# Kernel tuning notes

Measured on AMD Instinct MI355X. Metric: run time of the kernel, lower is better.

Reference implementation:

```python
import jax, jax.numpy as jnp
import numpy as np

N_NODES = 100000
N_EDGES = 1600000
N_GRAPHS = 1024
D = 128
L = 3
BN_EPS = 1e-5


def setup_inputs() -> dict:
    key = jax.random.key(0)
    ks = jax.random.split(key, 16)
    x = jax.random.normal(ks[0], (N_NODES, D), dtype=jnp.float32)
    edge_index = jax.random.randint(ks[1], (2, N_EDGES), 0, N_NODES, dtype=jnp.int64)
    batch = jnp.sort(jax.random.randint(ks[2], (N_NODES,), 0, N_GRAPHS, dtype=jnp.int64))
    w = lambda k, shape: jax.random.normal(k, shape, dtype=jnp.float32) * 0.05
    return {
        "x": x,
        "edge_index": edge_index,
        "batch": batch,
        "conv_W1": w(ks[3], (L, D, D)),
        "conv_b1": w(ks[4], (L, D)),
        "bn_gamma": jax.random.uniform(ks[5], (L, D), dtype=jnp.float32) + 0.5,
        "bn_beta": w(ks[6], (L, D)),
        "bn_mean": w(ks[7], (L, D)),
        "bn_var": jax.random.uniform(ks[8], (L, D), dtype=jnp.float32) + 0.5,
        "conv_W2": w(ks[9], (L, D, D)),
        "conv_b2": w(ks[10], (L, D)),
        "head_W1": w(ks[11], (D, D)),
        "head_b1": w(ks[12], (D,)),
        "head_W2": w(ks[13], (D, D)),
        "head_b2": w(ks[14], (D,)),
    }


def reference(x, edge_index, batch, conv_W1, conv_b1, bn_gamma, bn_beta,
              bn_mean, bn_var, conv_W2, conv_b2, head_W1, head_b1,
              head_W2, head_b2):
    n = x.shape[0]
    src, dst = edge_index[0], edge_index[1]
    for l in range(L):
        # GINConv, eps=0: nn(x + sum_{j->i} x_j)
        agg = jax.ops.segment_sum(x[src], dst, num_segments=n)  # [N, D]
        h = x + agg
        # MLP([in, h, h]): Linear -> BatchNorm(eval) -> ReLU -> Linear
        h = h @ conv_W1[l] + conv_b1[l]
        h = (h - bn_mean[l]) * jax.lax.rsqrt(bn_var[l] + BN_EPS) * bn_gamma[l] + bn_beta[l]
        h = jax.nn.relu(h)
        h = h @ conv_W2[l] + conv_b2[l]
        x = jax.nn.relu(h)  # .relu() in the outer forward
    # global_add_pool over graph ids
    g = jax.ops.segment_sum(x, batch, num_segments=N_GRAPHS)  # [B, D]
    # head MLP (norm=None, dropout inactive at eval): Linear -> ReLU -> Linear
    g = jax.nn.relu(g @ head_W1 + head_b1)
    return g @ head_W2 + head_b2
```

## Files before the change

kernel.cpp:

```cpp
#include <hip/hip_runtime.h>

#define N_NODES  100000
#define N_EDGES  1600000
#define N_GRAPHS 1024
#define D        128
#define BN_EPS   1e-5f

#define FNSLICE      98
#define FSLICE_NODES 1024
#define FSLICE_CAP   20480
#define QCAP         96
#define CCHUNK       4000
#define CGRID        400

#define CVT_BLOCKS   6250
#define PW_BLOCKS    384
#define FOLD_BLOCKS  3
#define GST_BLOCKS   5
#define MISC_BASE    (CVT_BLOCKS + PW_BLOCKS + FOLD_BLOCKS + GST_BLOCKS)
#define COMPACT_BASE (MISC_BASE + 1)
#define SETUP_GRID   (COMPACT_BASE + CGRID)

#define GATHER_GRID  12500

typedef short bf16x8 __attribute__((ext_vector_type(8)));
typedef float f32x4  __attribute__((ext_vector_type(4)));

__device__ __forceinline__ ushort f2bf(float f) {
    unsigned int b = __float_as_uint(f);
    return (ushort)((b + 0x7fffu + ((b >> 16) & 1u)) >> 16);
}
__device__ __forceinline__ float bflo(unsigned int u) { return __uint_as_float(u << 16); }
__device__ __forceinline__ float bfhi(unsigned int u) { return __uint_as_float(u & 0xffff0000u); }
__device__ __forceinline__ unsigned int packbf(float x, float y) {
    return (unsigned int)f2bf(x) | ((unsigned int)f2bf(y) << 16);
}

__global__ __launch_bounds__(256) void setup_kernel(
        const float* __restrict__ x, ushort* __restrict__ xb,
        const float* __restrict__ W1, const float* __restrict__ W2,
        ushort* __restrict__ Wt,
        const float* __restrict__ b1, const float* __restrict__ gamma,
        const float* __restrict__ beta, const float* __restrict__ mean,
        const float* __restrict__ var, const float* __restrict__ b2,
        float* __restrict__ folds,
        const int* __restrict__ batch, int* __restrict__ gstart,
        int* __restrict__ slice_tail, int* __restrict__ offsets,
        const int* __restrict__ src, const int* __restrict__ dst,
        unsigned int* __restrict__ squeue) {
    __shared__ unsigned int qbuf[FNSLICE * QCAP];
    __shared__ int qcnt[FNSLICE];
    __shared__ int qbase[FNSLICE];
    int b = blockIdx.x, t = threadIdx.x;
    if (b < CVT_BLOCKS) {
        size_t i = ((size_t)b * 256 + t) * 8;
        float4 v0 = *(const float4*)(x + i);
        float4 v1 = *(const float4*)(x + i + 4);
        uint4 o;
        o.x = packbf(v0.x, v0.y); o.y = packbf(v0.z, v0.w);
        o.z = packbf(v1.x, v1.y); o.w = packbf(v1.z, v1.w);
        *(uint4*)(xb + i) = o;
    } else if (b < CVT_BLOCKS + PW_BLOCKS) {
        int idx = (b - CVT_BLOCKS) * 256 + t;
        int i = idx >> 14, r = idx & 16383;
        int n = r >> 7, k = r & 127, l = i >> 1;
        const float* W = (i & 1) ? (W2 + (size_t)l * D * D) : (W1 + (size_t)l * D * D);
        Wt[idx] = f2bf(W[k * D + n]);
    } else if (b < CVT_BLOCKS + PW_BLOCKS + FOLD_BLOCKS) {
        int idx = (b - CVT_BLOCKS - PW_BLOCKS) * 256 + t;
        if (idx < 6 * D) {
            int i = idx >> 7, j = idx & 127, l = i >> 1;
            float s, o;
            if ((i & 1) == 0) {
                float sv = gamma[l * D + j] * rsqrtf(var[l * D + j] + BN_EPS);
                s = sv;
                o = (b1[l * D + j] - mean[l * D + j]) * sv + beta[l * D + j];
            } else {
                s = 1.0f;
                o = b2[l * D + j];
            }
            folds[(size_t)i * 2 * D + j]     = s;
            folds[(size_t)i * 2 * D + D + j] = o;
        }
    } else if (b < MISC_BASE) {
        int g = (b - CVT_BLOCKS - PW_BLOCKS - FOLD_BLOCKS) * 256 + t;
        if (g <= N_GRAPHS) {
            int lo = 0, hi = N_NODES;
            while (lo < hi) {
                int mid = (lo + hi) >> 1;
                if (batch[mid] < g) lo = mid + 1; else hi = mid;
            }
            gstart[g] = lo;
        }
    } else if (b == MISC_BASE) {
        if (t == 255) offsets[N_NODES] = N_EDGES;
    } else {
        for (int i = t; i < FNSLICE; i += 256) qcnt[i] = 0;
        __syncthreads();
        int e0 = (b - COMPACT_BASE) * CCHUNK;
        int eend = e0 + CCHUNK; if (eend > N_EDGES) eend = N_EDGES;
        for (int e = e0 + t; e < eend; e += 256) {
            int d = dst[e], s = src[e];
            int sl = d >> 10;
            unsigned int pk = ((unsigned int)(d & 1023) << 17) | (unsigned int)s;
            int pos = atomicAdd(&qcnt[sl], 1);
            if (pos < QCAP) qbuf[sl * QCAP + pos] = pk;
            else {
                int gp = atomicAdd(&slice_tail[sl], 1);
                squeue[(size_t)sl * FSLICE_CAP + gp] = pk;
            }
        }
        __syncthreads();
        for (int i = t; i < FNSLICE; i += 256) {
            int n = qcnt[i]; if (n > QCAP) n = QCAP;
            qbase[i] = atomicAdd(&slice_tail[i], n);
        }
        __syncthreads();
        int wv = t >> 6, ln = t & 63;
        for (int sl = wv; sl < FNSLICE; sl += 4) {
            int n = qcnt[sl]; if (n > QCAP) n = QCAP;
            int gb = qbase[sl];
            for (int i = ln; i < n; i += 64)
                squeue[(size_t)sl * FSLICE_CAP + gb + i] = qbuf[sl * QCAP + i];
        }
    }
}

__global__ __launch_bounds__(1024) void fill_local(const unsigned int* __restrict__ squeue,
                                                   const int* __restrict__ slice_tail,
                                                   int* __restrict__ offsets,
                                                   int* __restrict__ csr_src) {
    __shared__ int hist[FSLICE_NODES];
    __shared__ int cur[FSLICE_NODES];
    __shared__ int sbase[128];
    __shared__ int wsum[16];
    int sl = blockIdx.x, t = threadIdx.x;
    int n = slice_tail[sl];
    if (t < 128) sbase[t] = (t < FNSLICE) ? slice_tail[t] : 0;
    hist[t] = 0;
    __syncthreads();
    for (int off = 1; off < 128; off <<= 1) {
        int u = (t < 128 && t >= off) ? sbase[t - off] : 0;
        __syncthreads();
        if (t < 128) sbase[t] += u;
        __syncthreads();
    }
    int gbase = (sl == 0) ? 0 : sbase[sl - 1];
    size_t qb = (size_t)sl * FSLICE_CAP;
    for (int i = t; i < n; i += 1024)
        atomicAdd(&hist[squeue[qb + i] >> 17], 1);
    __syncthreads();
    int c = hist[t];
    int lane = t & 63, w = t >> 6;
    int sc = c;
#pragma unroll
    for (int off = 1; off < 64; off <<= 1) {
        int u = __shfl_up(sc, off, 64);
        if (lane >= off) sc += u;
    }
    if (lane == 63) wsum[w] = sc;
    __syncthreads();
    if (t < 16) {
        int ws = wsum[t];
        int s2 = ws;
#pragma unroll
        for (int off = 1; off < 16; off <<= 1) {
            int u = __shfl_up(s2, off, 16);
            if (t >= off) s2 += u;
        }
        wsum[t] = s2 - ws;
    }
    __syncthreads();
    int gslot = gbase + sc + wsum[w] - c;
    cur[t] = gslot;
    int node = sl * FSLICE_NODES + t;
    if (node < N_NODES) offsets[node] = gslot;
    __syncthreads();
    for (int i = t; i < n; i += 1024) {
        unsigned int p = squeue[qb + i];
        int slot = atomicAdd(&cur[p >> 17], 1);
        csr_src[slot] = (int)(p & 0x1FFFFu);
    }
}

__device__ __forceinline__ void drain_stream(const unsigned int* __restrict__ base,
                                             const int* __restrict__ csr,
                                             int i, int e, int lane,
                                             float& ax, float& ay) {
    for (; i + 15 < e; i += 16) {
        int s0 = csr[i],      s1 = csr[i + 1],  s2 = csr[i + 2],  s3 = csr[i + 3];
        int s4 = csr[i + 4],  s5 = csr[i + 5],  s6 = csr[i + 6],  s7 = csr[i + 7];
        int s8 = csr[i + 8],  s9 = csr[i + 9],  sa = csr[i + 10], sb = csr[i + 11];
        int sc = csr[i + 12], sd = csr[i + 13], se = csr[i + 14], sf = csr[i + 15];
        unsigned int v0 = base[(size_t)s0 * 64 + lane];
        unsigned int v1 = base[(size_t)s1 * 64 + lane];
        unsigned int v2 = base[(size_t)s2 * 64 + lane];
        unsigned int v3 = base[(size_t)s3 * 64 + lane];
        unsigned int v4 = base[(size_t)s4 * 64 + lane];
        unsigned int v5 = base[(size_t)s5 * 64 + lane];
        unsigned int v6 = base[(size_t)s6 * 64 + lane];
        unsigned int v7 = base[(size_t)s7 * 64 + lane];
        unsigned int v8 = base[(size_t)s8 * 64 + lane];
        unsigned int v9 = base[(size_t)s9 * 64 + lane];
        unsigned int va = base[(size_t)sa * 64 + lane];
        unsigned int vb = base[(size_t)sb * 64 + lane];
        unsigned int vc = base[(size_t)sc * 64 + lane];
        unsigned int vd = base[(size_t)sd * 64 + lane];
        unsigned int ve = base[(size_t)se * 64 + lane];
        unsigned int vf = base[(size_t)sf * 64 + lane];
        ax += bflo(v0) + bflo(v1) + bflo(v2) + bflo(v3)
            + bflo(v4) + bflo(v5) + bflo(v6) + bflo(v7)
            + bflo(v8) + bflo(v9) + bflo(va) + bflo(vb)
            + bflo(vc) + bflo(vd) + bflo(ve) + bflo(vf);
        ay += bfhi(v0) + bfhi(v1) + bfhi(v2) + bfhi(v3)
            + bfhi(v4) + bfhi(v5) + bfhi(v6) + bfhi(v7)
            + bfhi(v8) + bfhi(v9) + bfhi(va) + bfhi(vb)
            + bfhi(vc) + bfhi(vd) + bfhi(ve) + bfhi(vf);
    }
    for (; i + 3 < e; i += 4) {
        int s0 = csr[i], s1 = csr[i + 1], s2 = csr[i + 2], s3 = csr[i + 3];
        unsigned int v0 = base[(size_t)s0 * 64 + lane];
        unsigned int v1 = base[(size_t)s1 * 64 + lane];
        unsigned int v2 = base[(size_t)s2 * 64 + lane];
        unsigned int v3 = base[(size_t)s3 * 64 + lane];
        ax += bflo(v0) + bflo(v1) + bflo(v2) + bflo(v3);
        ay += bfhi(v0) + bfhi(v1) + bfhi(v2) + bfhi(v3);
    }
    for (; i < e; ++i) {
        unsigned int v = base[(size_t)csr[i] * 64 + lane];
        ax += bflo(v); ay += bfhi(v);
    }
}

__global__ __launch_bounds__(256) void gather_bf16(const ushort* __restrict__ xb,
                                                   const int* __restrict__ offsets,
                                                   const int* __restrict__ csr_src,
                                                   ushort* __restrict__ hb) {
    int wv = threadIdx.x >> 6, lane = threadIdx.x & 63;
    int n0 = (blockIdx.x * 4 + wv) * 2;
    const unsigned int* base = (const unsigned int*)xb;
    unsigned int u0 = base[(size_t)n0 * 64 + lane];
    unsigned int u1 = base[(size_t)(n0 + 1) * 64 + lane];
    float ax0 = bflo(u0), ay0 = bfhi(u0);
    float ax1 = bflo(u1), ay1 = bfhi(u1);
    int i0 = offsets[n0];
    int e0 = offsets[n0 + 1];
    int i1 = e0;
    int e1 = offsets[n0 + 2];
    while (i0 + 7 < e0 && i1 + 7 < e1) {
        int s0 = csr_src[i0],     s1 = csr_src[i0 + 1],
            s2 = csr_src[i0 + 2], s3 = csr_src[i0 + 3];
        int s4 = csr_src[i0 + 4], s5 = csr_src[i0 + 5],
            s6 = csr_src[i0 + 6], s7 = csr_src[i0 + 7];
        int r0 = csr_src[i1],     r1 = csr_src[i1 + 1],
            r2 = csr_src[i1 + 2], r3 = csr_src[i1 + 3];
        int r4 = csr_src[i1 + 4], r5 = csr_src[i1 + 5],
            r6 = csr_src[i1 + 6], r7 = csr_src[i1 + 7];
        unsigned int v0 = base[(size_t)s0 * 64 + lane];
        unsigned int v1 = base[(size_t)s1 * 64 + lane];
        unsigned int v2 = base[(size_t)s2 * 64 + lane];
        unsigned int v3 = base[(size_t)s3 * 64 + lane];
        unsigned int v4 = base[(size_t)s4 * 64 + lane];
        unsigned int v5 = base[(size_t)s5 * 64 + lane];
        unsigned int v6 = base[(size_t)s6 * 64 + lane];
        unsigned int v7 = base[(size_t)s7 * 64 + lane];
        unsigned int w0 = base[(size_t)r0 * 64 + lane];
        unsigned int w1 = base[(size_t)r1 * 64 + lane];
        unsigned int w2 = base[(size_t)r2 * 64 + lane];
        unsigned int w3 = base[(size_t)r3 * 64 + lane];
        unsigned int w4 = base[(size_t)r4 * 64 + lane];
        unsigned int w5 = base[(size_t)r5 * 64 + lane];
        unsigned int w6 = base[(size_t)r6 * 64 + lane];
        unsigned int w7 = base[(size_t)r7 * 64 + lane];
        ax0 += bflo(v0) + bflo(v1) + bflo(v2) + bflo(v3)
             + bflo(v4) + bflo(v5) + bflo(v6) + bflo(v7);
        ay0 += bfhi(v0) + bfhi(v1) + bfhi(v2) + bfhi(v3)
             + bfhi(v4) + bfhi(v5) + bfhi(v6) + bfhi(v7);
        ax1 += bflo(w0) + bflo(w1) + bflo(w2) + bflo(w3)
             + bflo(w4) + bflo(w5) + bflo(w6) + bflo(w7);
        ay1 += bfhi(w0) + bfhi(w1) + bfhi(w2) + bfhi(w3)
             + bfhi(w4) + bfhi(w5) + bfhi(w6) + bfhi(w7);
        i0 += 8; i1 += 8;
    }
    drain_stream(base, csr_src, i0, e0, lane, ax0, ay0);
    drain_stream(base, csr_src, i1, e1, lane, ax1, ay1);
    ((unsigned int*)hb)[(size_t)n0 * 64 + lane]       = packbf(ax0, ay0);
    ((unsigned int*)hb)[(size_t)(n0 + 1) * 64 + lane] = packbf(ax1, ay1);
}

__global__ __launch_bounds__(512, 4) void fused_gemm(const ushort* __restrict__ in,
                                                     ushort* __restrict__ out,
                                                     const ushort* __restrict__ Wt1,
                                                     const ushort* __restrict__ Wt2,
                                                     const float* __restrict__ fold1,
                                                     const float* __restrict__ fold2) {
    __shared__ ushort As[128 * 136];
    __shared__ ushort Bs[128 * 136];
    int t = threadIdx.x;
    int row0 = blockIdx.x * 128;

#pragma unroll
    for (int i = 0; i < 4; ++i) {
        int f = t + 512 * i; int m = f >> 4, g = f & 15;
        *(float4*)(As + m * 136 + g * 8) = *(const float4*)(in + (size_t)(row0 + m) * D + g * 8);
        *(float4*)(Bs + m * 136 + g * 8) = *(const float4*)(Wt1 + (size_t)m * D + g * 8);
    }
    const uint4* w2v = (const uint4*)Wt2;
    uint4 p0 = w2v[t];
    uint4 p1 = w2v[t + 512];
    uint4 p2 = w2v[t + 1024];
    uint4 p3 = w2v[t + 1536];
    __syncthreads();

    int lane = t & 63, wv = t >> 6;
    int quad = lane >> 4, mr = lane & 15;
    int mbase = wv * 16;
    const ushort* ap = As + (mbase + mr) * 136 + quad * 8;
    bf16x8 a0 = *(const bf16x8*)(ap);
    bf16x8 a1 = *(const bf16x8*)(ap + 32);
    bf16x8 a2 = *(const bf16x8*)(ap + 64);
    bf16x8 a3 = *(const bf16x8*)(ap + 96);

#pragma unroll
    for (int nt = 0; nt < 8; ++nt) {
        const ushort* bq = Bs + (nt * 16 + mr) * 136 + quad * 8;
        bf16x8 b0 = *(const bf16x8*)(bq);
        bf16x8 b1 = *(const bf16x8*)(bq + 32);
        bf16x8 b2 = *(const bf16x8*)(bq + 64);
        bf16x8 b3 = *(const bf16x8*)(bq + 96);
        f32x4 acc = {0.f, 0.f, 0.f, 0.f};
        acc = __builtin_amdgcn_mfma_f32_16x16x32_bf16(a0, b0, acc, 0, 0, 0);
        acc = __builtin_amdgcn_mfma_f32_16x16x32_bf16(a1, b1, acc, 0, 0, 0);
        acc = __builtin_amdgcn_mfma_f32_16x16x32_bf16(a2, b2, acc, 0, 0, 0);
        acc = __builtin_amdgcn_mfma_f32_16x16x32_bf16(a3, b3, acc, 0, 0, 0);
        int j = nt * 16 + mr;
        float s = fold1[j], o = fold1[D + j];
#pragma unroll
        for (int r = 0; r < 4; ++r) {
            float z = fmaxf(fmaf(acc[r], s, o), 0.0f);
            As[(mbase + quad * 4 + r) * 136 + j] = f2bf(z);
        }
    }
    __syncthreads();

    {
        int f0 = t;          *(uint4*)(Bs + (f0 >> 4) * 136 + (f0 & 15) * 8) = p0;
        int f1 = t + 512;    *(uint4*)(Bs + (f1 >> 4) * 136 + (f1 & 15) * 8) = p1;
        int f2 = t + 1024;   *(uint4*)(Bs + (f2 >> 4) * 136 + (f2 & 15) * 8) = p2;
        int f3 = t + 1536;   *(uint4*)(Bs + (f3 >> 4) * 136 + (f3 & 15) * 8) = p3;
    }
    const ushort* hp = As + (mbase + mr) * 136 + quad * 8;
    bf16x8 h0 = *(const bf16x8*)(hp);
    bf16x8 h1 = *(const bf16x8*)(hp + 32);
    bf16x8 h2 = *(const bf16x8*)(hp + 64);
    bf16x8 h3 = *(const bf16x8*)(hp + 96);
    __syncthreads();

#pragma unroll
    for (int nt = 0; nt < 8; ++nt) {
        const ushort* bq = Bs + (nt * 16 + mr) * 136 + quad * 8;
        bf16x8 b0 = *(const bf16x8*)(bq);
        bf16x8 b1 = *(const bf16x8*)(bq + 32);
        bf16x8 b2 = *(const bf16x8*)(bq + 64);
        bf16x8 b3 = *(const bf16x8*)(bq + 96);
        f32x4 acc = {0.f, 0.f, 0.f, 0.f};
        acc = __builtin_amdgcn_mfma_f32_16x16x32_bf16(h0, b0, acc, 0, 0, 0);
        acc = __builtin_amdgcn_mfma_f32_16x16x32_bf16(h1, b1, acc, 0, 0, 0);
        acc = __builtin_amdgcn_mfma_f32_16x16x32_bf16(h2, b2, acc, 0, 0, 0);
        acc = __builtin_amdgcn_mfma_f32_16x16x32_bf16(h3, b3, acc, 0, 0, 0);
        int j = nt * 16 + mr;
        float o = fold2[D + j];
#pragma unroll
        for (int r = 0; r < 4; ++r) {
            float z = fmaxf(acc[r] + o, 0.0f);
            As[(mbase + quad * 4 + r) * 136 + j] = f2bf(z);
        }
    }
    __syncthreads();

#pragma unroll
    for (int i = 0; i < 8; ++i) {
        int f = t + 512 * i; int lr = f >> 5, g = f & 31;
        if (row0 + lr < N_NODES)
            *(float2*)(out + (size_t)(row0 + lr) * D + g * 4) =
                *(const float2*)(As + lr * 136 + g * 4);
    }
}

__global__ __launch_bounds__(128) void poolhead_kernel(const ushort* __restrict__ xb,
                                                       const int* __restrict__ gstart,
                                                       const float* __restrict__ W1,
                                                       const float* __restrict__ b1,
                                                       const float* __restrict__ W2,
                                                       const float* __restrict__ b2,
                                                       float* __restrict__ out) {
    __shared__ float row[128];
    __shared__ float t1[128];
    int r = blockIdx.x, j = threadIdx.x;
    float acc = 0.0f;
    int b = gstart[r], e = gstart[r + 1];
    for (int i = b; i < e; ++i)
        acc += __uint_as_float(((unsigned int)xb[(size_t)i * D + j]) << 16);
    row[j] = acc;
    __syncthreads();
    float a1 = b1[j];
    for (int k = 0; k < D; ++k) a1 = fmaf(row[k], W1[k * D + j], a1);
    t1[j] = fmaxf(a1, 0.0f);
    __syncthreads();
    float a2 = b2[j];
    for (int k = 0; k < D; ++k) a2 = fmaf(t1[k], W2[k * D + j], a2);
    out[r * D + j] = a2;
}

extern "C" void kernel_launch(void* const* d_in, const int* in_sizes, int n_in,
                              void* d_out, int out_size, void* d_ws, size_t ws_size,
                              hipStream_t stream) {
    const float* x        = (const float*)d_in[0];
    const int*   ei       = (const int*)d_in[1];
    const int*   src      = ei;
    const int*   dst      = ei + N_EDGES;
    const int*   batch    = (const int*)d_in[2];
    const float* conv_W1  = (const float*)d_in[3];
    const float* conv_b1  = (const float*)d_in[4];
    const float* bn_gamma = (const float*)d_in[5];
    const float* bn_beta  = (const float*)d_in[6];
    const float* bn_mean  = (const float*)d_in[7];
    const float* bn_var   = (const float*)d_in[8];
    const float* conv_W2  = (const float*)d_in[9];
    const float* conv_b2  = (const float*)d_in[10];
    const float* head_W1  = (const float*)d_in[11];
    const float* head_b1  = (const float*)d_in[12];
    const float* head_W2  = (const float*)d_in[13];
    const float* head_b2  = (const float*)d_in[14];
    float* out = (float*)d_out;

    char* ws = (char*)d_ws;
    size_t off = 0;
    auto alloc = [&](size_t bytes) -> void* {
        void* p = ws + off;
        off = (off + bytes + 255) & ~(size_t)255;
        return p;
    };
    const size_t NODE_BUF = (size_t)(N_NODES + 128) * D * sizeof(ushort);
    ushort* buf0    = (ushort*)alloc(NODE_BUF);
    ushort* buf1    = (ushort*)alloc(NODE_BUF);
    ushort* Wt      = (ushort*)alloc((size_t)6 * D * D * sizeof(ushort));
    float*  folds   = (float*)alloc((size_t)6 * 2 * D * sizeof(float));
    unsigned int* squeue = (unsigned int*)alloc((size_t)FNSLICE * FSLICE_CAP * sizeof(unsigned int));
    int*   csr_src  = (int*)alloc((size_t)(N_EDGES + 64) * sizeof(int));
    int*   offsets  = (int*)alloc((size_t)(N_NODES + 1) * sizeof(int));
    int*   slice_tail = (int*)alloc((size_t)FNSLICE * sizeof(int));
    int*   gstart   = (int*)alloc((size_t)(N_GRAPHS + 1) * sizeof(int));

    hipMemsetAsync(slice_tail, 0, FNSLICE * sizeof(int), stream);
    setup_kernel<<<SETUP_GRID, 256, 0, stream>>>(
        x, buf0, conv_W1, conv_W2, Wt,
        conv_b1, bn_gamma, bn_beta, bn_mean, bn_var, conv_b2, folds,
        batch, gstart, slice_tail, offsets, src, dst, squeue);
    fill_local<<<FNSLICE, 1024, 0, stream>>>(squeue, slice_tail, offsets, csr_src);

    const int FUSED_GRID = (N_NODES + 127) / 128;
    for (int l = 0; l < 3; ++l) {
        gather_bf16<<<GATHER_GRID, 256, 0, stream>>>(buf0, offsets, csr_src, buf1);
        fused_gemm<<<FUSED_GRID, 512, 0, stream>>>(buf1, buf0,
            Wt + (size_t)(2 * l) * D * D, Wt + (size_t)(2 * l + 1) * D * D,
            folds + (size_t)(2 * l) * 2 * D, folds + (size_t)(2 * l + 1) * 2 * D);
    }

    poolhead_kernel<<<N_GRAPHS, 128, 0, stream>>>(buf0, gstart, head_W1, head_b1,
                                                  head_W2, head_b2, out);
}
```

Baseline: 439.6 us.

## Fuse global add pooling into last layer GEMM epilogue via atomics

The last GIN layer's GEMM now accumulates its output rows directly into a per-graph pool buffer with run-length segmented sums and float atomics, instead of writing node features and reading them back in the pool/head kernel. The setup kernel zeroes the pool buffer instead of binary-searching graph start offsets, and the head kernel just reads pooled rows. This removes the final node-feature write and reread and the serial per-graph reduction loop. In exchange it adds atomic contention and makes the float summation order nondeterministic.

```diff
diff --git a/kernel.cpp b/kernel.cpp
--- a/kernel.cpp
+++ b/kernel.cpp
@@ -16,8 +16,9 @@
 #define CVT_BLOCKS   6250
 #define PW_BLOCKS    384
 #define FOLD_BLOCKS  3
-#define GST_BLOCKS   5
-#define MISC_BASE    (CVT_BLOCKS + PW_BLOCKS + FOLD_BLOCKS + GST_BLOCKS)
+#define PZ_BLOCKS    128
+#define PZ_BASE      (CVT_BLOCKS + PW_BLOCKS + FOLD_BLOCKS)
+#define MISC_BASE    (PZ_BASE + PZ_BLOCKS)
 #define COMPACT_BASE (MISC_BASE + 1)
 #define SETUP_GRID   (COMPACT_BASE + CGRID)
 
@@ -43,8 +44,7 @@
         const float* __restrict__ b1, const float* __restrict__ gamma,
         const float* __restrict__ beta, const float* __restrict__ mean,
         const float* __restrict__ var, const float* __restrict__ b2,
-        float* __restrict__ folds,
-        const int* __restrict__ batch, int* __restrict__ gstart,
+        float* __restrict__ folds, float* __restrict__ pool,
         int* __restrict__ slice_tail, int* __restrict__ offsets,
         const int* __restrict__ src, const int* __restrict__ dst,
         unsigned int* __restrict__ squeue) {
@@ -66,7 +66,7 @@
         int n = r >> 7, k = r & 127, l = i >> 1;
         const float* W = (i & 1) ? (W2 + (size_t)l * D * D) : (W1 + (size_t)l * D * D);
         Wt[idx] = f2bf(W[k * D + n]);
-    } else if (b < CVT_BLOCKS + PW_BLOCKS + FOLD_BLOCKS) {
+    } else if (b < PZ_BASE) {
         int idx = (b - CVT_BLOCKS - PW_BLOCKS) * 256 + t;
         if (idx < 6 * D) {
             int i = idx >> 7, j = idx & 127, l = i >> 1;
@@ -83,15 +83,8 @@
             folds[(size_t)i * 2 * D + D + j] = o;
         }
     } else if (b < MISC_BASE) {
-        int g = (b - CVT_BLOCKS - PW_BLOCKS - FOLD_BLOCKS) * 256 + t;
-        if (g <= N_GRAPHS) {
-            int lo = 0, hi = N_NODES;
-            while (lo < hi) {
-                int mid = (lo + hi) >> 1;
-                if (batch[mid] < g) lo = mid + 1; else hi = mid;
-            }
-            gstart[g] = lo;
-        }
+        int idx = (b - PZ_BASE) * 256 + t;
+        ((float4*)pool)[idx] = float4{0.f, 0.f, 0.f, 0.f};
     } else if (b == MISC_BASE) {
         if (t == 255) offsets[N_NODES] = N_EDGES;
     } else {
@@ -387,21 +380,131 @@
     }
 }
 
-__global__ __launch_bounds__(128) void poolhead_kernel(const ushort* __restrict__ xb,
-                                                       const int* __restrict__ gstart,
-                                                       const float* __restrict__ W1,
-                                                       const float* __restrict__ b1,
-                                                       const float* __restrict__ W2,
-                                                       const float* __restrict__ b2,
-                                                       float* __restrict__ out) {
+__global__ __launch_bounds__(512, 4) void fused_gemm_pool(const ushort* __restrict__ in,
+                                                          const int* __restrict__ batch,
+                                                          float* __restrict__ pool,
+                                                          const ushort* __restrict__ Wt1,
+                                                          const ushort* __restrict__ Wt2,
+                                                          const float* __restrict__ fold1,
+                                                          const float* __restrict__ fold2) {
+    __shared__ ushort As[128 * 136];
+    __shared__ ushort Bs[128 * 136];
+    __shared__ int bb[128];
+    int t = threadIdx.x;
+    int row0 = blockIdx.x * 128;
+
+#pragma unroll
+    for (int i = 0; i < 4; ++i) {
+        int f = t + 512 * i; int m = f >> 4, g = f & 15;
+        *(float4*)(As + m * 136 + g * 8) = *(const float4*)(in + (size_t)(row0 + m) * D + g * 8);
+        *(float4*)(Bs + m * 136 + g * 8) = *(const float4*)(Wt1 + (size_t)m * D + g * 8);
+    }
+    const uint4* w2v = (const uint4*)Wt2;
+    uint4 p0 = w2v[t];
+    uint4 p1 = w2v[t + 512];
+    uint4 p2 = w2v[t + 1024];
+    uint4 p3 = w2v[t + 1536];
+    __syncthreads();
+
+    int lane = t & 63, wv = t >> 6;
+    int quad = lane >> 4, mr = lane & 15;
+    int mbase = wv * 16;
+    const ushort* ap = As + (mbase + mr) * 136 + quad * 8;
+    bf16x8 a0 = *(const bf16x8*)(ap);
+    bf16x8 a1 = *(const bf16x8*)(ap + 32);
+    bf16x8 a2 = *(const bf16x8*)(ap + 64);
+    bf16x8 a3 = *(const bf16x8*)(ap + 96);
+
+#pragma unroll
+    for (int nt = 0; nt < 8; ++nt) {
+        const ushort* bq = Bs + (nt * 16 + mr) * 136 + quad * 8;
+        bf16x8 b0 = *(const bf16x8*)(bq);
+        bf16x8 b1 = *(const bf16x8*)(bq + 32);
+        bf16x8 b2 = *(const bf16x8*)(bq + 64);
+        bf16x8 b3 = *(const bf16x8*)(bq + 96);
+        f32x4 acc = {0.f, 0.f, 0.f, 0.f};
+        acc = __builtin_amdgcn_mfma_f32_16x16x32_bf16(a0, b0, acc, 0, 0, 0);
+        acc = __builtin_amdgcn_mfma_f32_16x16x32_bf16(a1, b1, acc, 0, 0, 0);
+        acc = __builtin_amdgcn_mfma_f32_16x16x32_bf16(a2, b2, acc, 0, 0, 0);
+        acc = __builtin_amdgcn_mfma_f32_16x16x32_bf16(a3, b3, acc, 0, 0, 0);
+        int j = nt * 16 + mr;
+        float s = fold1[j], o = fold1[D + j];
+#pragma unroll
+        for (int r = 0; r < 4; ++r) {
+            float z = fmaxf(fmaf(acc[r], s, o), 0.0f);
+            As[(mbase + quad * 4 + r) * 136 + j] = f2bf(z);
+        }
+    }
+    __syncthreads();
+
+    {
+        int f0 = t;          *(uint4*)(Bs + (f0 >> 4) * 136 + (f0 & 15) * 8) = p0;
+        int f1 = t + 512;    *(uint4*)(Bs + (f1 >> 4) * 136 + (f1 & 15) * 8) = p1;
+        int f2 = t + 1024;   *(uint4*)(Bs + (f2 >> 4) * 136 + (f2 & 15) * 8) = p2;
+        int f3 = t + 1536;   *(uint4*)(Bs + (f3 >> 4) * 136 + (f3 & 15) * 8) = p3;
+    }
+    const ushort* hp = As + (mbase + mr) * 136 + quad * 8;
+    bf16x8 h0 = *(const bf16x8*)(hp);
+    bf16x8 h1 = *(const bf16x8*)(hp + 32);
+    bf16x8 h2 = *(const bf16x8*)(hp + 64);
+    bf16x8 h3 = *(const bf16x8*)(hp + 96);
+    __syncthreads();
+
+#pragma unroll
+    for (int nt = 0; nt < 8; ++nt) {
+        const ushort* bq = Bs + (nt * 16 + mr) * 136 + quad * 8;
+        bf16x8 b0 = *(const bf16x8*)(bq);
+        bf16x8 b1 = *(const bf16x8*)(bq + 32);
+        bf16x8 b2 = *(const bf16x8*)(bq + 64);
+        bf16x8 b3 = *(const bf16x8*)(bq + 96);
+        f32x4 acc = {0.f, 0.f, 0.f, 0.f};
+        acc = __builtin_amdgcn_mfma_f32_16x16x32_bf16(h0, b0, acc, 0, 0, 0);
+        acc = __builtin_amdgcn_mfma_f32_16x16x32_bf16(h1, b1, acc, 0, 0, 0);
+        acc = __builtin_amdgcn_mfma_f32_16x16x32_bf16(h2, b2, acc, 0, 0, 0);
+        acc = __builtin_amdgcn_mfma_f32_16x16x32_bf16(h3, b3, acc, 0, 0, 0);
+        int j = nt * 16 + mr;
+        float o = fold2[D + j];
+#pragma unroll
+        for (int r = 0; r < 4; ++r) {
+            float z = fmaxf(acc[r] + o, 0.0f);
+            As[(mbase + quad * 4 + r) * 136 + j] = f2bf(z);
+        }
+    }
+    if (t < 128)
+        bb[t] = (row0 + t < N_NODES) ? batch[row0 + t] : -1;
+    __syncthreads();
+
+    {
+        int j = t & 127, rg = t >> 7;
+        int rbeg = rg * 32;
+        if (row0 + rbeg < N_NODES) {
+            int curg = bb[rbeg];
+            float s = 0.0f;
+#pragma unroll 1
+            for (int r = rbeg; r < rbeg + 32; ++r) {
+                if (row0 + r >= N_NODES) break;
+                int g = bb[r];
+                if (g != curg) {
+                    atomicAdd(pool + (size_t)curg * D + j, s);
+                    s = 0.0f; curg = g;
+                }
+                s += __uint_as_float((unsigned int)As[r * 136 + j] << 16);
+            }
+            atomicAdd(pool + (size_t)curg * D + j, s);
+        }
+    }
+}
+
+__global__ __launch_bounds__(128) void head_kernel(const float* __restrict__ pool,
+                                                   const float* __restrict__ W1,
+                                                   const float* __restrict__ b1,
+                                                   const float* __restrict__ W2,
+                                                   const float* __restrict__ b2,
+                                                   float* __restrict__ out) {
     __shared__ float row[128];
     __shared__ float t1[128];
     int r = blockIdx.x, j = threadIdx.x;
-    float acc = 0.0f;
-    int b = gstart[r], e = gstart[r + 1];
-    for (int i = b; i < e; ++i)
-        acc += __uint_as_float(((unsigned int)xb[(size_t)i * D + j]) << 16);
-    row[j] = acc;
+    row[j] = pool[(size_t)r * D + j];
     __syncthreads();
     float a1 = b1[j];
     for (int k = 0; k < D; ++k) a1 = fmaf(row[k], W1[k * D + j], a1);
@@ -450,23 +553,27 @@
     int*   csr_src  = (int*)alloc((size_t)(N_EDGES + 64) * sizeof(int));
     int*   offsets  = (int*)alloc((size_t)(N_NODES + 1) * sizeof(int));
     int*   slice_tail = (int*)alloc((size_t)FNSLICE * sizeof(int));
-    int*   gstart   = (int*)alloc((size_t)(N_GRAPHS + 1) * sizeof(int));
+    float* pool     = (float*)alloc((size_t)N_GRAPHS * D * sizeof(float));
 
     hipMemsetAsync(slice_tail, 0, FNSLICE * sizeof(int), stream);
     setup_kernel<<<SETUP_GRID, 256, 0, stream>>>(
         x, buf0, conv_W1, conv_W2, Wt,
-        conv_b1, bn_gamma, bn_beta, bn_mean, bn_var, conv_b2, folds,
-        batch, gstart, slice_tail, offsets, src, dst, squeue);
+        conv_b1, bn_gamma, bn_beta, bn_mean, bn_var, conv_b2, folds, pool,
+        slice_tail, offsets, src, dst, squeue);
     fill_local<<<FNSLICE, 1024, 0, stream>>>(squeue, slice_tail, offsets, csr_src);
 
     const int FUSED_GRID = (N_NODES + 127) / 128;
-    for (int l = 0; l < 3; ++l) {
+    for (int l = 0; l < 2; ++l) {
         gather_bf16<<<GATHER_GRID, 256, 0, stream>>>(buf0, offsets, csr_src, buf1);
         fused_gemm<<<FUSED_GRID, 512, 0, stream>>>(buf1, buf0,
             Wt + (size_t)(2 * l) * D * D, Wt + (size_t)(2 * l + 1) * D * D,
             folds + (size_t)(2 * l) * 2 * D, folds + (size_t)(2 * l + 1) * 2 * D);
     }
-
-    poolhead_kernel<<<N_GRAPHS, 128, 0, stream>>>(buf0, gstart, head_W1, head_b1,
-                                                  head_W2, head_b2, out);
-}
+    gather_bf16<<<GATHER_GRID, 256, 0, stream>>>(buf0, offsets, csr_src, buf1);
+    fused_gemm_pool<<<FUSED_GRID, 512, 0, stream>>>(buf1, batch, pool,
+        Wt + (size_t)4 * D * D, Wt + (size_t)5 * D * D,
+        folds + (size_t)4 * 2 * D, folds + (size_t)5 * 2 * D);
+
+    head_kernel<<<N_GRAPHS, 128, 0, stream>>>(pool, head_W1, head_b1,
+                                              head_W2, head_b2, out);
+}
```

Result: faster. 411.4 us (-6.4%).
